# Kernel tuning notes

Measured on AMD Instinct MI355X. Metric: run time of the kernel, lower is better.

## Reference

```python
import jax, jax.numpy as jnp
import numpy as np

B, H, T, D = 4, 16, 2048, 64


def setup_inputs() -> dict:
    key = jax.random.key(0)
    kq, kk, kv = jax.random.split(key, 3)
    q = jax.random.normal(kq, (B, H, T, D), dtype=jnp.float32)
    k = jax.random.normal(kk, (B, H, T, D), dtype=jnp.float32)
    v = jax.random.normal(kv, (B, H, T, D), dtype=jnp.float32)
    return {"q": q, "k": k, "v": v}


def reference(q, k, v):
    # scores: [B,H,T,T] = q @ k^T (no softmax, linear attention)
    scores = jnp.einsum("bhtd,bhsd->bhts", q, k)
    # causal multiplicative mask: lower-triangular ones (zero out future keys)
    t = q.shape[-2]
    causal = jnp.tril(jnp.ones((t, t), dtype=scores.dtype))  # [T,T]
    scores = scores * causal  # broadcast over [B,H]
    # output: [B,H,T,D] = masked_scores @ v
    return jnp.einsum("bhts,bhsd->bhtd", scores, v)
```

## Files before the change

kernel.cpp:

```cpp
#include <hip/hip_runtime.h>
#include <hip/hip_bf16.h>


#define T_   2048
#define D_   64
#define CCH  128
#define NCH  16
#define LW   72

typedef __bf16 bf16x8 __attribute__((ext_vector_type(8)));
typedef __bf16 bf16x4 __attribute__((ext_vector_type(4)));
typedef float  f32x4  __attribute__((ext_vector_type(4)));


__device__ inline bf16x8 pack8(float4 a, float4 b) {
  bf16x8 r;
  r[0] = (__bf16)a.x; r[1] = (__bf16)a.y; r[2] = (__bf16)a.z; r[3] = (__bf16)a.w;
  r[4] = (__bf16)b.x; r[5] = (__bf16)b.y; r[6] = (__bf16)b.z; r[7] = (__bf16)b.w;
  return r;
}

__global__ __launch_bounds__(256, 4) void state_kernel(
    const float* __restrict__ k, const float* __restrict__ v,
    __bf16* __restrict__ stws) {
  __shared__ __align__(16) __bf16 KT[64][LW];
  __shared__ __align__(16) __bf16 VT[64][LW];

  const int tid  = threadIdx.x;
  const int lane = tid & 63;
  const int w    = tid >> 6;
  const int quad = lane >> 4;
  const int l15  = lane & 15;
  const int bh   = (int)blockIdx.x >> 4;
  const int c    = (int)blockIdx.x & (NCH - 1);
  if (c == NCH - 1) return;
  const long base = ((long)bh * T_ + (long)c * CCH) * D_;
  const int d0   = w * 16;

  const f32x4 vzero = {0.f, 0.f, 0.f, 0.f};
  f32x4 st[4];
#pragma unroll
  for (int n = 0; n < 4; ++n) st[n] = vzero;

  for (int j = 0; j < 2; ++j) {
    if (j) __syncthreads();
    {
      const float* krow = k + base + (long)(j * 64 + lane) * D_ + d0;
      const float* vrow = v + base + (long)(j * 64 + lane) * D_ + d0;
      float4 k0 = *(const float4*)(krow + 0),  k1 = *(const float4*)(krow + 4);
      float4 k2 = *(const float4*)(krow + 8),  k3 = *(const float4*)(krow + 12);
      float4 v0 = *(const float4*)(vrow + 0),  v1 = *(const float4*)(vrow + 4);
      float4 v2 = *(const float4*)(vrow + 8),  v3 = *(const float4*)(vrow + 12);
      KT[d0 +  0][lane] = (__bf16)k0.x; KT[d0 +  1][lane] = (__bf16)k0.y;
      KT[d0 +  2][lane] = (__bf16)k0.z; KT[d0 +  3][lane] = (__bf16)k0.w;
      KT[d0 +  4][lane] = (__bf16)k1.x; KT[d0 +  5][lane] = (__bf16)k1.y;
      KT[d0 +  6][lane] = (__bf16)k1.z; KT[d0 +  7][lane] = (__bf16)k1.w;
      KT[d0 +  8][lane] = (__bf16)k2.x; KT[d0 +  9][lane] = (__bf16)k2.y;
      KT[d0 + 10][lane] = (__bf16)k2.z; KT[d0 + 11][lane] = (__bf16)k2.w;
      KT[d0 + 12][lane] = (__bf16)k3.x; KT[d0 + 13][lane] = (__bf16)k3.y;
      KT[d0 + 14][lane] = (__bf16)k3.z; KT[d0 + 15][lane] = (__bf16)k3.w;
      VT[d0 +  0][lane] = (__bf16)v0.x; VT[d0 +  1][lane] = (__bf16)v0.y;
      VT[d0 +  2][lane] = (__bf16)v0.z; VT[d0 +  3][lane] = (__bf16)v0.w;
      VT[d0 +  4][lane] = (__bf16)v1.x; VT[d0 +  5][lane] = (__bf16)v1.y;
      VT[d0 +  6][lane] = (__bf16)v1.z; VT[d0 +  7][lane] = (__bf16)v1.w;
      VT[d0 +  8][lane] = (__bf16)v2.x; VT[d0 +  9][lane] = (__bf16)v2.y;
      VT[d0 + 10][lane] = (__bf16)v2.z; VT[d0 + 11][lane] = (__bf16)v2.w;
      VT[d0 + 12][lane] = (__bf16)v3.x; VT[d0 + 13][lane] = (__bf16)v3.y;
      VT[d0 + 14][lane] = (__bf16)v3.z; VT[d0 + 15][lane] = (__bf16)v3.w;
    }
    __syncthreads();
    bf16x8 ka0 = *(const bf16x8*)&KT[d0 + l15][quad * 8];
    bf16x8 ka1 = *(const bf16x8*)&KT[d0 + l15][32 + quad * 8];
#pragma unroll
    for (int n = 0; n < 4; ++n) {
      bf16x8 b0 = *(const bf16x8*)&VT[n * 16 + l15][quad * 8];
      bf16x8 b1 = *(const bf16x8*)&VT[n * 16 + l15][32 + quad * 8];
      st[n] = __builtin_amdgcn_mfma_f32_16x16x32_bf16(ka0, b0, st[n], 0, 0, 0);
      st[n] = __builtin_amdgcn_mfma_f32_16x16x32_bf16(ka1, b1, st[n], 0, 0, 0);
    }
  }
  __bf16* wsp = stws + ((long)blockIdx.x << 12);
#pragma unroll
  for (int n = 0; n < 4; ++n) {
    bf16x4 pk;
    pk[0] = (__bf16)st[n][0]; pk[1] = (__bf16)st[n][1];
    pk[2] = (__bf16)st[n][2]; pk[3] = (__bf16)st[n][3];
    *(bf16x4*)&wsp[(n * 16 + l15) * 64 + d0 + quad * 4] = pk;
  }
}

__global__ __launch_bounds__(64) void scan_kernel(
    const __bf16* __restrict__ st, __bf16* __restrict__ cum) {
  const int t  = threadIdx.x;
  const int bh = (int)blockIdx.x >> 3;
  const int sl = (int)blockIdx.x & 7;
  const long sbase = ((long)bh * NCH) << 12;
  const int off = sl * 512 + t * 8;

  float acc[8];
#pragma unroll
  for (int i = 0; i < 8; ++i) acc[i] = 0.f;

  bf16x8 cur = *(const bf16x8*)(st + sbase + off);
  for (int c = 0; c < NCH - 1; ++c) {
    bf16x8 nxt;
    if (c + 1 < NCH - 1)
      nxt = *(const bf16x8*)(st + sbase + ((long)(c + 1) << 12) + off);
#pragma unroll
    for (int i = 0; i < 8; ++i) acc[i] += (float)cur[i];
    bf16x8 o;
#pragma unroll
    for (int i = 0; i < 8; ++i) o[i] = (__bf16)acc[i];
    *(bf16x8*)(cum + sbase + ((long)c << 12) + off) = o;
    cur = nxt;
  }
}

__global__ __launch_bounds__(256, 4) void attn_kernel(
    const float* __restrict__ q, const float* __restrict__ k,
    const float* __restrict__ v, const __bf16* __restrict__ cum,
    float* __restrict__ out) {
  __shared__ __align__(16) __bf16 Kj[64][LW];
  __shared__ __align__(16) __bf16 VT[64][LW];
  __shared__ __align__(16) __bf16 Sw[4][2][16][LW];

  const int tid  = threadIdx.x;
  const int lane = tid & 63;
  const int w    = tid >> 6;
  const int quad = lane >> 4;
  const int l15  = lane & 15;
  const int bh   = (int)blockIdx.x >> 4;
  const int c    = (int)blockIdx.x & (NCH - 1);
  const long base = ((long)bh * T_ + (long)c * CCH) * D_;
  const int d0   = w * 16;

  {
    const float* krow = k + base + (long)lane * D_ + d0;
    const float* vrow = v + base + (long)lane * D_ + d0;
    float4 k0 = *(const float4*)(krow + 0),  k1 = *(const float4*)(krow + 4);
    float4 k2 = *(const float4*)(krow + 8),  k3 = *(const float4*)(krow + 12);
    float4 v0 = *(const float4*)(vrow + 0),  v1 = *(const float4*)(vrow + 4);
    float4 v2 = *(const float4*)(vrow + 8),  v3 = *(const float4*)(vrow + 12);
    *(bf16x8*)&Kj[lane][d0]     = pack8(k0, k1);
    *(bf16x8*)&Kj[lane][d0 + 8] = pack8(k2, k3);
    VT[d0 +  0][lane] = (__bf16)v0.x; VT[d0 +  1][lane] = (__bf16)v0.y;
    VT[d0 +  2][lane] = (__bf16)v0.z; VT[d0 +  3][lane] = (__bf16)v0.w;
    VT[d0 +  4][lane] = (__bf16)v1.x; VT[d0 +  5][lane] = (__bf16)v1.y;
    VT[d0 +  6][lane] = (__bf16)v1.z; VT[d0 +  7][lane] = (__bf16)v1.w;
    VT[d0 +  8][lane] = (__bf16)v2.x; VT[d0 +  9][lane] = (__bf16)v2.y;
    VT[d0 + 10][lane] = (__bf16)v2.z; VT[d0 + 11][lane] = (__bf16)v2.w;
    VT[d0 + 12][lane] = (__bf16)v3.x; VT[d0 + 13][lane] = (__bf16)v3.y;
    VT[d0 + 14][lane] = (__bf16)v3.z; VT[d0 + 15][lane] = (__bf16)v3.w;
  }

  bf16x8 qf[2][2];
#pragma unroll
  for (int i = 0; i < 2; ++i) {
    const float* qp = q + base + (long)((w + 4 * i) * 16 + l15) * D_ + quad * 8;
#pragma unroll
    for (int ks = 0; ks < 2; ++ks)
      qf[i][ks] = pack8(*(const float4*)(qp + ks * 32),
                        *(const float4*)(qp + ks * 32 + 4));
  }

  bf16x8 kvf[2][4];
  if (c) {
    const __bf16* cp = cum + ((long)(bh * NCH + (c - 1)) << 12);
#pragma unroll
    for (int ks = 0; ks < 2; ++ks)
#pragma unroll
      for (int n = 0; n < 4; ++n)
        kvf[ks][n] =
            *(const bf16x8*)(cp + (n * 16 + l15) * 64 + ks * 32 + quad * 8);
  }

  const f32x4 vzero = {0.f, 0.f, 0.f, 0.f};
  f32x4 acc[2][4];
#pragma unroll
  for (int i = 0; i < 2; ++i)
#pragma unroll
    for (int n = 0; n < 4; ++n) acc[i][n] = vzero;

  __syncthreads();

  if (c) {
#pragma unroll
    for (int ks = 0; ks < 2; ++ks)
#pragma unroll
      for (int n = 0; n < 4; ++n) {
        acc[0][n] = __builtin_amdgcn_mfma_f32_16x16x32_bf16(qf[0][ks], kvf[ks][n], acc[0][n], 0, 0, 0);
        acc[1][n] = __builtin_amdgcn_mfma_f32_16x16x32_bf16(qf[1][ks], kvf[ks][n], acc[1][n], 0, 0, 0);
      }
  }

  bf16x8 vb[2][4];
#pragma unroll
  for (int ks = 0; ks < 2; ++ks)
#pragma unroll
    for (int n = 0; n < 4; ++n)
      vb[ks][n] = *(const bf16x8*)&VT[n * 16 + l15][ks * 32 + quad * 8];

  f32x4 sA[4], sB[4];
#pragma unroll
  for (int n = 0; n < 4; ++n) { sA[n] = vzero; sB[n] = vzero; }
#pragma unroll
  for (int ks = 0; ks < 2; ++ks)
#pragma unroll
    for (int n = 0; n < 4; ++n) {
      bf16x8 bK = *(const bf16x8*)&Kj[n * 16 + l15][ks * 32 + quad * 8];
      sA[n] = __builtin_amdgcn_mfma_f32_16x16x32_bf16(qf[0][ks], bK, sA[n], 0, 0, 0);
      sB[n] = __builtin_amdgcn_mfma_f32_16x16x32_bf16(qf[1][ks], bK, sB[n], 0, 0, 0);
    }

  __bf16* sw0 = &Sw[w][0][0][0];
  __bf16* sw1 = &Sw[w][1][0][0];

#pragma unroll
  for (int n = 0; n < 4; ++n)
#pragma unroll
    for (int rr = 0; rr < 4; ++rr) {
      float val = sA[n][rr];
      if (n * 16 + l15 > 16 * w + quad * 4 + rr) val = 0.f;
      sw0[(quad * 4 + rr) * LW + n * 16 + l15] = (__bf16)val;
    }
#pragma unroll
  for (int n = 0; n < 4; ++n)
#pragma unroll
    for (int rr = 0; rr < 4; ++rr)
      sw1[(quad * 4 + rr) * LW + n * 16 + l15] = (__bf16)sB[n][rr];

  {
    bf16x8 a0 = *(const bf16x8*)&sw0[l15 * LW + quad * 8];
    bf16x8 a1 = *(const bf16x8*)&sw0[l15 * LW + 32 + quad * 8];
    bf16x8 b0 = *(const bf16x8*)&sw1[l15 * LW + quad * 8];
    bf16x8 b1 = *(const bf16x8*)&sw1[l15 * LW + 32 + quad * 8];
#pragma unroll
    for (int n = 0; n < 4; ++n) {
      acc[0][n] = __builtin_amdgcn_mfma_f32_16x16x32_bf16(a0, vb[0][n], acc[0][n], 0, 0, 0);
      acc[0][n] = __builtin_amdgcn_mfma_f32_16x16x32_bf16(a1, vb[1][n], acc[0][n], 0, 0, 0);
      acc[1][n] = __builtin_amdgcn_mfma_f32_16x16x32_bf16(b0, vb[0][n], acc[1][n], 0, 0, 0);
      acc[1][n] = __builtin_amdgcn_mfma_f32_16x16x32_bf16(b1, vb[1][n], acc[1][n], 0, 0, 0);
    }
  }

  __syncthreads();

  {
    const float* krow = k + base + (long)(64 + lane) * D_ + d0;
    const float* vrow = v + base + (long)(64 + lane) * D_ + d0;
    float4 k0 = *(const float4*)(krow + 0),  k1 = *(const float4*)(krow + 4);
    float4 k2 = *(const float4*)(krow + 8),  k3 = *(const float4*)(krow + 12);
    float4 v0 = *(const float4*)(vrow + 0),  v1 = *(const float4*)(vrow + 4);
    float4 v2 = *(const float4*)(vrow + 8),  v3 = *(const float4*)(vrow + 12);
    *(bf16x8*)&Kj[lane][d0]     = pack8(k0, k1);
    *(bf16x8*)&Kj[lane][d0 + 8] = pack8(k2, k3);
    VT[d0 +  0][lane] = (__bf16)v0.x; VT[d0 +  1][lane] = (__bf16)v0.y;
    VT[d0 +  2][lane] = (__bf16)v0.z; VT[d0 +  3][lane] = (__bf16)v0.w;
    VT[d0 +  4][lane] = (__bf16)v1.x; VT[d0 +  5][lane] = (__bf16)v1.y;
    VT[d0 +  6][lane] = (__bf16)v1.z; VT[d0 +  7][lane] = (__bf16)v1.w;
    VT[d0 +  8][lane] = (__bf16)v2.x; VT[d0 +  9][lane] = (__bf16)v2.y;
    VT[d0 + 10][lane] = (__bf16)v2.z; VT[d0 + 11][lane] = (__bf16)v2.w;
    VT[d0 + 12][lane] = (__bf16)v3.x; VT[d0 + 13][lane] = (__bf16)v3.y;
    VT[d0 + 14][lane] = (__bf16)v3.z; VT[d0 + 15][lane] = (__bf16)v3.w;
  }
  __syncthreads();

#pragma unroll
  for (int ks = 0; ks < 2; ++ks)
#pragma unroll
    for (int n = 0; n < 4; ++n)
      vb[ks][n] = *(const bf16x8*)&VT[n * 16 + l15][ks * 32 + quad * 8];

  f32x4 sC[4];
#pragma unroll
  for (int n = 0; n < 4; ++n) sC[n] = vzero;
#pragma unroll
  for (int ks = 0; ks < 2; ++ks)
#pragma unroll
    for (int n = 0; n < 4; ++n) {
      bf16x8 bK = *(const bf16x8*)&Kj[n * 16 + l15][ks * 32 + quad * 8];
      sC[n] = __builtin_amdgcn_mfma_f32_16x16x32_bf16(qf[1][ks], bK, sC[n], 0, 0, 0);
    }
#pragma unroll
  for (int n = 0; n < 4; ++n)
#pragma unroll
    for (int rr = 0; rr < 4; ++rr) {
      float val = sC[n][rr];
      if (n * 16 + l15 > 16 * w + quad * 4 + rr) val = 0.f;
      sw0[(quad * 4 + rr) * LW + n * 16 + l15] = (__bf16)val;
    }
  {
    bf16x8 a0 = *(const bf16x8*)&sw0[l15 * LW + quad * 8];
    bf16x8 a1 = *(const bf16x8*)&sw0[l15 * LW + 32 + quad * 8];
#pragma unroll
    for (int n = 0; n < 4; ++n) {
      acc[1][n] = __builtin_amdgcn_mfma_f32_16x16x32_bf16(a0, vb[0][n], acc[1][n], 0, 0, 0);
      acc[1][n] = __builtin_amdgcn_mfma_f32_16x16x32_bf16(a1, vb[1][n], acc[1][n], 0, 0, 0);
    }
  }

  float* op = out + base;
#pragma unroll
  for (int i = 0; i < 2; ++i) {
    int row = (w + 4 * i) * 16 + quad * 4;
#pragma unroll
    for (int n = 0; n < 4; ++n)
#pragma unroll
      for (int rr = 0; rr < 4; ++rr)
        op[(long)(row + rr) * D_ + n * 16 + l15] = acc[i][n][rr];
  }
}

extern "C" void kernel_launch(void* const* d_in, const int* in_sizes, int n_in,
                              void* d_out, int out_size, void* d_ws, size_t ws_size,
                              hipStream_t stream) {
  const float* q = (const float*)d_in[0];
  const float* k = (const float*)d_in[1];
  const float* v = (const float*)d_in[2];
  float* out = (float*)d_out;
  __bf16* stws = (__bf16*)d_ws;
  __bf16* cum  = stws + ((long)64 * NCH << 12);

  hipLaunchKernelGGL(state_kernel, dim3(64 * NCH), dim3(256), 0, stream,
                     k, v, stws);
  hipLaunchKernelGGL(scan_kernel, dim3(64 * 8), dim3(64), 0, stream,
                     stws, cum);
  hipLaunchKernelGGL(attn_kernel, dim3(64 * NCH), dim3(256), 0, stream,
                     q, k, v, cum, out);
}
```

Before: 158.3 us.

## Hoist all global loads up front and drop mid-kernel LDS staging of K

The state kernel now loads both 64-row halves of K and V before a single barrier and keeps them in double-sized LDS buffers. The scan kernel issues all chunk loads before the sequential prefix sum. The attention kernel reads K fragments straight from global memory into registers, stages both V halves at once, and removes the two mid-kernel barriers and the second LDS fill. The aim is more memory-level parallelism and fewer synchronisations, at the cost of more registers and LDS, which may lower occupancy.

```diff
diff --git a/kernel.cpp b/kernel.cpp
--- a/kernel.cpp
+++ b/kernel.cpp
@@ -23,8 +23,8 @@
 __global__ __launch_bounds__(256, 4) void state_kernel(
     const float* __restrict__ k, const float* __restrict__ v,
     __bf16* __restrict__ stws) {
-  __shared__ __align__(16) __bf16 KT[64][LW];
-  __shared__ __align__(16) __bf16 VT[64][LW];
+  __shared__ __align__(16) __bf16 KT[2][64][LW];
+  __shared__ __align__(16) __bf16 VT[2][64][LW];
 
   const int tid  = threadIdx.x;
   const int lane = tid & 63;
@@ -37,44 +37,45 @@
   const long base = ((long)bh * T_ + (long)c * CCH) * D_;
   const int d0   = w * 16;
 
+  float4 kx[2][4], vx[2][4];
+#pragma unroll
+  for (int j = 0; j < 2; ++j) {
+    const float* krow = k + base + (long)(j * 64 + lane) * D_ + d0;
+    const float* vrow = v + base + (long)(j * 64 + lane) * D_ + d0;
+#pragma unroll
+    for (int x = 0; x < 4; ++x) {
+      kx[j][x] = *(const float4*)(krow + x * 4);
+      vx[j][x] = *(const float4*)(vrow + x * 4);
+    }
+  }
+#pragma unroll
+  for (int j = 0; j < 2; ++j)
+#pragma unroll
+    for (int x = 0; x < 4; ++x) {
+      int dd = d0 + x * 4;
+      KT[j][dd + 0][lane] = (__bf16)kx[j][x].x;
+      KT[j][dd + 1][lane] = (__bf16)kx[j][x].y;
+      KT[j][dd + 2][lane] = (__bf16)kx[j][x].z;
+      KT[j][dd + 3][lane] = (__bf16)kx[j][x].w;
+      VT[j][dd + 0][lane] = (__bf16)vx[j][x].x;
+      VT[j][dd + 1][lane] = (__bf16)vx[j][x].y;
+      VT[j][dd + 2][lane] = (__bf16)vx[j][x].z;
+      VT[j][dd + 3][lane] = (__bf16)vx[j][x].w;
+    }
+  __syncthreads();
+
   const f32x4 vzero = {0.f, 0.f, 0.f, 0.f};
   f32x4 st[4];
 #pragma unroll
   for (int n = 0; n < 4; ++n) st[n] = vzero;
-
+#pragma unroll
   for (int j = 0; j < 2; ++j) {
-    if (j) __syncthreads();
-    {
-      const float* krow = k + base + (long)(j * 64 + lane) * D_ + d0;
-      const float* vrow = v + base + (long)(j * 64 + lane) * D_ + d0;
-      float4 k0 = *(const float4*)(krow + 0),  k1 = *(const float4*)(krow + 4);
-      float4 k2 = *(const float4*)(krow + 8),  k3 = *(const float4*)(krow + 12);
-      float4 v0 = *(const float4*)(vrow + 0),  v1 = *(const float4*)(vrow + 4);
-      float4 v2 = *(const float4*)(vrow + 8),  v3 = *(const float4*)(vrow + 12);
-      KT[d0 +  0][lane] = (__bf16)k0.x; KT[d0 +  1][lane] = (__bf16)k0.y;
-      KT[d0 +  2][lane] = (__bf16)k0.z; KT[d0 +  3][lane] = (__bf16)k0.w;
-      KT[d0 +  4][lane] = (__bf16)k1.x; KT[d0 +  5][lane] = (__bf16)k1.y;
-      KT[d0 +  6][lane] = (__bf16)k1.z; KT[d0 +  7][lane] = (__bf16)k1.w;
-      KT[d0 +  8][lane] = (__bf16)k2.x; KT[d0 +  9][lane] = (__bf16)k2.y;
-      KT[d0 + 10][lane] = (__bf16)k2.z; KT[d0 + 11][lane] = (__bf16)k2.w;
-      KT[d0 + 12][lane] = (__bf16)k3.x; KT[d0 + 13][lane] = (__bf16)k3.y;
-      KT[d0 + 14][lane] = (__bf16)k3.z; KT[d0 + 15][lane] = (__bf16)k3.w;
-      VT[d0 +  0][lane] = (__bf16)v0.x; VT[d0 +  1][lane] = (__bf16)v0.y;
-      VT[d0 +  2][lane] = (__bf16)v0.z; VT[d0 +  3][lane] = (__bf16)v0.w;
-      VT[d0 +  4][lane] = (__bf16)v1.x; VT[d0 +  5][lane] = (__bf16)v1.y;
-      VT[d0 +  6][lane] = (__bf16)v1.z; VT[d0 +  7][lane] = (__bf16)v1.w;
-      VT[d0 +  8][lane] = (__bf16)v2.x; VT[d0 +  9][lane] = (__bf16)v2.y;
-      VT[d0 + 10][lane] = (__bf16)v2.z; VT[d0 + 11][lane] = (__bf16)v2.w;
-      VT[d0 + 12][lane] = (__bf16)v3.x; VT[d0 + 13][lane] = (__bf16)v3.y;
-      VT[d0 + 14][lane] = (__bf16)v3.z; VT[d0 + 15][lane] = (__bf16)v3.w;
-    }
-    __syncthreads();
-    bf16x8 ka0 = *(const bf16x8*)&KT[d0 + l15][quad * 8];
-    bf16x8 ka1 = *(const bf16x8*)&KT[d0 + l15][32 + quad * 8];
-#pragma unroll
-    for (int n = 0; n < 4; ++n) {
-      bf16x8 b0 = *(const bf16x8*)&VT[n * 16 + l15][quad * 8];
-      bf16x8 b1 = *(const bf16x8*)&VT[n * 16 + l15][32 + quad * 8];
+    bf16x8 ka0 = *(const bf16x8*)&KT[j][d0 + l15][quad * 8];
+    bf16x8 ka1 = *(const bf16x8*)&KT[j][d0 + l15][32 + quad * 8];
+#pragma unroll
+    for (int n = 0; n < 4; ++n) {
+      bf16x8 b0 = *(const bf16x8*)&VT[j][n * 16 + l15][quad * 8];
+      bf16x8 b1 = *(const bf16x8*)&VT[j][n * 16 + l15][32 + quad * 8];
       st[n] = __builtin_amdgcn_mfma_f32_16x16x32_bf16(ka0, b0, st[n], 0, 0, 0);
       st[n] = __builtin_amdgcn_mfma_f32_16x16x32_bf16(ka1, b1, st[n], 0, 0, 0);
     }
@@ -97,22 +98,22 @@
   const long sbase = ((long)bh * NCH) << 12;
   const int off = sl * 512 + t * 8;
 
+  bf16x8 ch[NCH - 1];
+#pragma unroll
+  for (int c = 0; c < NCH - 1; ++c)
+    ch[c] = *(const bf16x8*)(st + sbase + ((long)c << 12) + off);
+
   float acc[8];
 #pragma unroll
   for (int i = 0; i < 8; ++i) acc[i] = 0.f;
-
-  bf16x8 cur = *(const bf16x8*)(st + sbase + off);
+#pragma unroll
   for (int c = 0; c < NCH - 1; ++c) {
-    bf16x8 nxt;
-    if (c + 1 < NCH - 1)
-      nxt = *(const bf16x8*)(st + sbase + ((long)(c + 1) << 12) + off);
-#pragma unroll
-    for (int i = 0; i < 8; ++i) acc[i] += (float)cur[i];
+#pragma unroll
+    for (int i = 0; i < 8; ++i) acc[i] += (float)ch[c][i];
     bf16x8 o;
 #pragma unroll
     for (int i = 0; i < 8; ++i) o[i] = (__bf16)acc[i];
     *(bf16x8*)(cum + sbase + ((long)c << 12) + off) = o;
-    cur = nxt;
   }
 }
 
@@ -120,8 +121,7 @@
     const float* __restrict__ q, const float* __restrict__ k,
     const float* __restrict__ v, const __bf16* __restrict__ cum,
     float* __restrict__ out) {
-  __shared__ __align__(16) __bf16 Kj[64][LW];
-  __shared__ __align__(16) __bf16 VT[64][LW];
+  __shared__ __align__(16) __bf16 VT[2][64][LW];
   __shared__ __align__(16) __bf16 Sw[4][2][16][LW];
 
   const int tid  = threadIdx.x;
@@ -134,25 +134,13 @@
   const long base = ((long)bh * T_ + (long)c * CCH) * D_;
   const int d0   = w * 16;
 
-  {
-    const float* krow = k + base + (long)lane * D_ + d0;
-    const float* vrow = v + base + (long)lane * D_ + d0;
-    float4 k0 = *(const float4*)(krow + 0),  k1 = *(const float4*)(krow + 4);
-    float4 k2 = *(const float4*)(krow + 8),  k3 = *(const float4*)(krow + 12);
-    float4 v0 = *(const float4*)(vrow + 0),  v1 = *(const float4*)(vrow + 4);
-    float4 v2 = *(const float4*)(vrow + 8),  v3 = *(const float4*)(vrow + 12);
-    *(bf16x8*)&Kj[lane][d0]     = pack8(k0, k1);
-    *(bf16x8*)&Kj[lane][d0 + 8] = pack8(k2, k3);
-    VT[d0 +  0][lane] = (__bf16)v0.x; VT[d0 +  1][lane] = (__bf16)v0.y;
-    VT[d0 +  2][lane] = (__bf16)v0.z; VT[d0 +  3][lane] = (__bf16)v0.w;
-    VT[d0 +  4][lane] = (__bf16)v1.x; VT[d0 +  5][lane] = (__bf16)v1.y;
-    VT[d0 +  6][lane] = (__bf16)v1.z; VT[d0 +  7][lane] = (__bf16)v1.w;
-    VT[d0 +  8][lane] = (__bf16)v2.x; VT[d0 +  9][lane] = (__bf16)v2.y;
-    VT[d0 + 10][lane] = (__bf16)v2.z; VT[d0 + 11][lane] = (__bf16)v2.w;
-    VT[d0 + 12][lane] = (__bf16)v3.x; VT[d0 + 13][lane] = (__bf16)v3.y;
-    VT[d0 + 14][lane] = (__bf16)v3.z; VT[d0 + 15][lane] = (__bf16)v3.w;
-  }
-
+  float4 vx[2][4];
+#pragma unroll
+  for (int j = 0; j < 2; ++j) {
+    const float* vrow = v + base + (long)(j * 64 + lane) * D_ + d0;
+#pragma unroll
+    for (int x = 0; x < 4; ++x) vx[j][x] = *(const float4*)(vrow + x * 4);
+  }
   bf16x8 qf[2][2];
 #pragma unroll
   for (int i = 0; i < 2; ++i) {
@@ -162,7 +150,6 @@
       qf[i][ks] = pack8(*(const float4*)(qp + ks * 32),
                         *(const float4*)(qp + ks * 32 + 4));
   }
-
   bf16x8 kvf[2][4];
   if (c) {
     const __bf16* cp = cum + ((long)(bh * NCH + (c - 1)) << 12);
@@ -173,6 +160,25 @@
         kvf[ks][n] =
             *(const bf16x8*)(cp + (n * 16 + l15) * 64 + ks * 32 + quad * 8);
   }
+  bf16x8 kf0[2][4];
+#pragma unroll
+  for (int ks = 0; ks < 2; ++ks)
+#pragma unroll
+    for (int n = 0; n < 4; ++n) {
+      const float* kp = k + base + (long)(n * 16 + l15) * D_ + ks * 32 + quad * 8;
+      kf0[ks][n] = pack8(*(const float4*)kp, *(const float4*)(kp + 4));
+    }
+
+#pragma unroll
+  for (int j = 0; j < 2; ++j)
+#pragma unroll
+    for (int x = 0; x < 4; ++x) {
+      int dd = d0 + x * 4;
+      VT[j][dd + 0][lane] = (__bf16)vx[j][x].x;
+      VT[j][dd + 1][lane] = (__bf16)vx[j][x].y;
+      VT[j][dd + 2][lane] = (__bf16)vx[j][x].z;
+      VT[j][dd + 3][lane] = (__bf16)vx[j][x].w;
+    }
 
   const f32x4 vzero = {0.f, 0.f, 0.f, 0.f};
   f32x4 acc[2][4];
@@ -182,6 +188,16 @@
     for (int n = 0; n < 4; ++n) acc[i][n] = vzero;
 
   __syncthreads();
+
+  bf16x8 kf1[2][4];
+#pragma unroll
+  for (int ks = 0; ks < 2; ++ks)
+#pragma unroll
+    for (int n = 0; n < 4; ++n) {
+      const float* kp =
+          k + base + (long)(64 + n * 16 + l15) * D_ + ks * 32 + quad * 8;
+      kf1[ks][n] = pack8(*(const float4*)kp, *(const float4*)(kp + 4));
+    }
 
   if (c) {
 #pragma unroll
@@ -198,7 +214,7 @@
   for (int ks = 0; ks < 2; ++ks)
 #pragma unroll
     for (int n = 0; n < 4; ++n)
-      vb[ks][n] = *(const bf16x8*)&VT[n * 16 + l15][ks * 32 + quad * 8];
+      vb[ks][n] = *(const bf16x8*)&VT[0][n * 16 + l15][ks * 32 + quad * 8];
 
   f32x4 sA[4], sB[4];
 #pragma unroll
@@ -207,14 +223,12 @@
   for (int ks = 0; ks < 2; ++ks)
 #pragma unroll
     for (int n = 0; n < 4; ++n) {
-      bf16x8 bK = *(const bf16x8*)&Kj[n * 16 + l15][ks * 32 + quad * 8];
-      sA[n] = __builtin_amdgcn_mfma_f32_16x16x32_bf16(qf[0][ks], bK, sA[n], 0, 0, 0);
-      sB[n] = __builtin_amdgcn_mfma_f32_16x16x32_bf16(qf[1][ks], bK, sB[n], 0, 0, 0);
+      sA[n] = __builtin_amdgcn_mfma_f32_16x16x32_bf16(qf[0][ks], kf0[ks][n], sA[n], 0, 0, 0);
+      sB[n] = __builtin_amdgcn_mfma_f32_16x16x32_bf16(qf[1][ks], kf0[ks][n], sB[n], 0, 0, 0);
     }
 
   __bf16* sw0 = &Sw[w][0][0][0];
   __bf16* sw1 = &Sw[w][1][0][0];
-
 #pragma unroll
   for (int n = 0; n < 4; ++n)
 #pragma unroll
@@ -222,13 +236,8 @@
       float val = sA[n][rr];
       if (n * 16 + l15 > 16 * w + quad * 4 + rr) val = 0.f;
       sw0[(quad * 4 + rr) * LW + n * 16 + l15] = (__bf16)val;
-    }
-#pragma unroll
-  for (int n = 0; n < 4; ++n)
-#pragma unroll
-    for (int rr = 0; rr < 4; ++rr)
       sw1[(quad * 4 + rr) * LW + n * 16 + l15] = (__bf16)sB[n][rr];
-
+    }
   {
     bf16x8 a0 = *(const bf16x8*)&sw0[l15 * LW + quad * 8];
     bf16x8 a1 = *(const bf16x8*)&sw0[l15 * LW + 32 + quad * 8];
@@ -243,33 +252,11 @@
     }
   }
 
-  __syncthreads();
-
-  {
-    const float* krow = k + base + (long)(64 + lane) * D_ + d0;
-    const float* vrow = v + base + (long)(64 + lane) * D_ + d0;
-    float4 k0 = *(const float4*)(krow + 0),  k1 = *(const float4*)(krow + 4);
-    float4 k2 = *(const float4*)(krow + 8),  k3 = *(const float4*)(krow + 12);
-    float4 v0 = *(const float4*)(vrow + 0),  v1 = *(const float4*)(vrow + 4);
-    float4 v2 = *(const float4*)(vrow + 8),  v3 = *(const float4*)(vrow + 12);
-    *(bf16x8*)&Kj[lane][d0]     = pack8(k0, k1);
-    *(bf16x8*)&Kj[lane][d0 + 8] = pack8(k2, k3);
-    VT[d0 +  0][lane] = (__bf16)v0.x; VT[d0 +  1][lane] = (__bf16)v0.y;
-    VT[d0 +  2][lane] = (__bf16)v0.z; VT[d0 +  3][lane] = (__bf16)v0.w;
-    VT[d0 +  4][lane] = (__bf16)v1.x; VT[d0 +  5][lane] = (__bf16)v1.y;
-    VT[d0 +  6][lane] = (__bf16)v1.z; VT[d0 +  7][lane] = (__bf16)v1.w;
-    VT[d0 +  8][lane] = (__bf16)v2.x; VT[d0 +  9][lane] = (__bf16)v2.y;
-    VT[d0 + 10][lane] = (__bf16)v2.z; VT[d0 + 11][lane] = (__bf16)v2.w;
-    VT[d0 + 12][lane] = (__bf16)v3.x; VT[d0 + 13][lane] = (__bf16)v3.y;
-    VT[d0 + 14][lane] = (__bf16)v3.z; VT[d0 + 15][lane] = (__bf16)v3.w;
-  }
-  __syncthreads();
-
 #pragma unroll
   for (int ks = 0; ks < 2; ++ks)
 #pragma unroll
     for (int n = 0; n < 4; ++n)
-      vb[ks][n] = *(const bf16x8*)&VT[n * 16 + l15][ks * 32 + quad * 8];
+      vb[ks][n] = *(const bf16x8*)&VT[1][n * 16 + l15][ks * 32 + quad * 8];
 
   f32x4 sC[4];
 #pragma unroll
@@ -277,10 +264,8 @@
 #pragma unroll
   for (int ks = 0; ks < 2; ++ks)
 #pragma unroll
-    for (int n = 0; n < 4; ++n) {
-      bf16x8 bK = *(const bf16x8*)&Kj[n * 16 + l15][ks * 32 + quad * 8];
-      sC[n] = __builtin_amdgcn_mfma_f32_16x16x32_bf16(qf[1][ks], bK, sC[n], 0, 0, 0);
-    }
+    for (int n = 0; n < 4; ++n)
+      sC[n] = __builtin_amdgcn_mfma_f32_16x16x32_bf16(qf[1][ks], kf1[ks][n], sC[n], 0, 0, 0);
 #pragma unroll
   for (int n = 0; n < 4; ++n)
 #pragma unroll
@@ -319,12 +304,12 @@
   const float* v = (const float*)d_in[2];
   float* out = (float*)d_out;
   __bf16* stws = (__bf16*)d_ws;
-  __bf16* cum  = stws + ((long)64 * NCH << 12);
+  __bf16* cumw = stws + ((long)64 * NCH << 12);
 
   hipLaunchKernelGGL(state_kernel, dim3(64 * NCH), dim3(256), 0, stream,
                      k, v, stws);
   hipLaunchKernelGGL(scan_kernel, dim3(64 * 8), dim3(64), 0, stream,
-                     stws, cum);
+                     stws, cumw);
   hipLaunchKernelGGL(attn_kernel, dim3(64 * NCH), dim3(256), 0, stream,
-                     q, k, v, cum, out);
-}
+                     q, k, v, cumw, out);
+}
```

Result: slower. 204.5 us (+29.1%).
